# Optimization experiments

Measured on AMD Instinct MI355X. Metric: run time of the kernel, lower is better.

The kernel has to match this reference:

```python
import jax, jax.numpy as jnp
import numpy as np

D_MODEL = 1024
NUM_HEADS = 16
HEAD_DIM = D_MODEL // NUM_HEADS


def setup_inputs() -> dict:
    key = jax.random.key(0)
    ks = jax.random.split(key, 11)
    B, S = 4, 2048
    s = 1.0 / np.sqrt(D_MODEL)
    inp = {
        'query': jax.random.normal(ks[0], (B, S, D_MODEL), jnp.float32),
        'key': jax.random.normal(ks[1], (B, S, D_MODEL), jnp.float32),
        'value': jax.random.normal(ks[2], (B, S, D_MODEL), jnp.float32),
        'W_q': jax.random.normal(ks[3], (D_MODEL, D_MODEL), jnp.float32) * s,
        'b_q': jnp.zeros((D_MODEL,), jnp.float32),
        'W_k': jax.random.normal(ks[4], (D_MODEL, D_MODEL), jnp.float32) * s,
        'b_k': jnp.zeros((D_MODEL,), jnp.float32),
        'W_v': jax.random.normal(ks[5], (D_MODEL, D_MODEL), jnp.float32) * s,
        'b_v': jnp.zeros((D_MODEL,), jnp.float32),
        'W_o': jax.random.normal(ks[6], (D_MODEL, D_MODEL), jnp.float32) * s,
        'b_o': jnp.zeros((D_MODEL,), jnp.float32),
    }
    return inp


def reference(query, key, value, W_q, b_q, W_k, b_k, W_v, b_v, W_o, b_o):
    B, S, _ = query.shape
    # Linear projections (torch Linear: x @ W.T + b)
    Q = query @ W_q.T + b_q
    K = key @ W_k.T + b_k
    V = value @ W_v.T + b_v
    # [B, H, S, Dh]
    def split_heads(x):
        return x.reshape(B, -1, NUM_HEADS, HEAD_DIM).transpose(0, 2, 1, 3)
    Qh, Kh, Vh = split_heads(Q), split_heads(K), split_heads(V)
    scale = 1.0 / jnp.sqrt(jnp.float32(HEAD_DIM))
    scores = jnp.einsum('bhqd,bhkd->bhqk', Qh, Kh) * scale
    attn = jax.nn.softmax(scores, axis=-1)
    out = jnp.einsum('bhqk,bhkd->bhqd', attn, Vh)
    out = out.transpose(0, 2, 1, 3).reshape(B, S, D_MODEL)
    return out @ W_o.T + b_o
```

## Files before the change

kernel.cpp:

```cpp
#include <hip/hip_runtime.h>


#define BATCH 4
#define SEQ   2048
#define NH    16
#define DH    64
#define DM    1024
#define LOG2E 1.4426950408889634f
#define CSC   (0.125f * LOG2E)

typedef __attribute__((ext_vector_type(8))) short s16x8;
typedef __attribute__((ext_vector_type(4))) float f32x4;
typedef __attribute__((ext_vector_type(4))) unsigned int u32x4;
typedef const __attribute__((address_space(1))) unsigned int* gas1;
typedef __attribute__((address_space(3))) unsigned int* las3;

__device__ __forceinline__ unsigned short f2bf(float f) {
  unsigned int u = __float_as_uint(f);
  u += 0x7FFFu + ((u >> 16) & 1u);
  return (unsigned short)(u >> 16);
}

__device__ __forceinline__ unsigned int cvt_pk_bf16(float lo, float hi) {
  unsigned int r;
  asm("v_cvt_pk_bf16_f32 %0, %1, %2" : "=v"(r) : "v"(lo), "v"(hi));
  return r;
}

__device__ __forceinline__ f32x4 vmax4(f32x4 a, f32x4 b) {
  f32x4 r;
  r[0] = fmaxf(a[0], b[0]); r[1] = fmaxf(a[1], b[1]);
  r[2] = fmaxf(a[2], b[2]); r[3] = fmaxf(a[3], b[3]);
  return r;
}

__global__ __launch_bounds__(256) void cvt3_k(const float* __restrict__ s0,
                                              const float* __restrict__ s1,
                                              const float* __restrict__ s2,
                                              unsigned short* __restrict__ d0,
                                              unsigned short* __restrict__ d1,
                                              unsigned short* __restrict__ d2, int n4) {
  const float* s = blockIdx.y == 0 ? s0 : blockIdx.y == 1 ? s1 : s2;
  unsigned short* d = blockIdx.y == 0 ? d0 : blockIdx.y == 1 ? d1 : d2;
  int i = blockIdx.x * 256 + threadIdx.x;
  if (i < n4) {
    float4 v = ((const float4*)s)[i];
    ushort4 o;
    o.x = f2bf(v.x); o.y = f2bf(v.y); o.z = f2bf(v.z); o.w = f2bf(v.w);
    ((ushort4*)d)[i] = o;
  }
}

__global__ __launch_bounds__(256) void cvt4_k(const float* __restrict__ s0,
                                              const float* __restrict__ s1,
                                              const float* __restrict__ s2,
                                              const float* __restrict__ s3,
                                              unsigned short* __restrict__ d0,
                                              unsigned short* __restrict__ d1,
                                              unsigned short* __restrict__ d2,
                                              unsigned short* __restrict__ d3, int n4) {
  const float* s = blockIdx.y == 0 ? s0 : blockIdx.y == 1 ? s1 : blockIdx.y == 2 ? s2 : s3;
  unsigned short* d = blockIdx.y == 0 ? d0 : blockIdx.y == 1 ? d1 : blockIdx.y == 2 ? d2 : d3;
  int i = blockIdx.x * 256 + threadIdx.x;
  if (i < n4) {
    float4 v = ((const float4*)s)[i];
    ushort4 o;
    o.x = f2bf(v.x); o.y = f2bf(v.y); o.z = f2bf(v.z); o.w = f2bf(v.w);
    ((ushort4*)d)[i] = o;
  }
}

template<bool BIAS_ROW, bool OUT_F32>
__device__ __forceinline__ void gemm_core(const unsigned short* __restrict__ A,
                                          const unsigned short* __restrict__ Bm,
                                          const float* __restrict__ bias,
                                          void* __restrict__ Cout,
                                          int M, int N, int K, int tM, int tN,
                                          unsigned short* As, unsigned short* Bs) {
  const int tid = threadIdx.x;
  const int wave = tid >> 6, lane = tid & 63;
  const int lr = lane & 15, lh = lane >> 4;
  const int wm = (wave >> 1) * 64, wn = (wave & 1) * 64;
  f32x4 acc[4][4] = {};

  for (int k0 = 0; k0 < K; k0 += 64) {
    __syncthreads();
#pragma unroll
    for (int i = 0; i < 4; ++i) {
      const int slot = wave * 256 + i * 64 + lane;
      const int row = slot >> 3;
      const int cg = (slot & 7) ^ (row & 7);
      const unsigned short* ga = A  + (size_t)(tM * 128 + row) * K + k0 + cg * 8;
      const unsigned short* gb = Bm + (size_t)(tN * 128 + row) * K + k0 + cg * 8;
      __builtin_amdgcn_global_load_lds((gas1)ga, (las3)(As + (wave * 256 + i * 64) * 8), 16, 0, 0);
      __builtin_amdgcn_global_load_lds((gas1)gb, (las3)(Bs + (wave * 256 + i * 64) * 8), 16, 0, 0);
    }
    __syncthreads();

    s16x8 af[4][2], bfr[4][2];
#pragma unroll
    for (int mt = 0; mt < 4; ++mt) {
#pragma unroll
      for (int kt = 0; kt < 2; ++kt) {
        const int ra = wm + mt * 16 + lr;
        af[mt][kt] = *(const s16x8*)(As + ra * 64 + (((kt * 4 + lh) ^ (ra & 7)) * 8));
        const int rb = wn + mt * 16 + lr;
        bfr[mt][kt] = *(const s16x8*)(Bs + rb * 64 + (((kt * 4 + lh) ^ (rb & 7)) * 8));
      }
    }
#pragma unroll
    for (int mt = 0; mt < 4; ++mt) {
#pragma unroll
      for (int nt = 0; nt < 4; ++nt) {
        acc[mt][nt] = __builtin_amdgcn_mfma_f32_16x16x32_bf16(af[mt][0], bfr[nt][0], acc[mt][nt], 0, 0, 0);
        acc[mt][nt] = __builtin_amdgcn_mfma_f32_16x16x32_bf16(af[mt][1], bfr[nt][1], acc[mt][nt], 0, 0, 0);
      }
    }
  }

#pragma unroll
  for (int mt = 0; mt < 4; ++mt) {
#pragma unroll
    for (int nt = 0; nt < 4; ++nt) {
      const int row0 = tM * 128 + wm + mt * 16 + lh * 4;
      const int col  = tN * 128 + wn + nt * 16 + lr;
      const float bc = BIAS_ROW ? 0.f : bias[col];
#pragma unroll
      for (int r = 0; r < 4; ++r) {
        const float v = acc[mt][nt][r] + (BIAS_ROW ? bias[row0 + r] : bc);
        if (OUT_F32) ((float*)Cout)[(size_t)(row0 + r) * N + col] = v;
        else ((unsigned short*)Cout)[(size_t)(row0 + r) * N + col] = f2bf(v);
      }
    }
  }
}

template<bool BIAS_ROW, bool OUT_F32>
__global__ __launch_bounds__(256) void gemm_bt(const unsigned short* __restrict__ A,
                                               const unsigned short* __restrict__ Bm,
                                               const float* __restrict__ bias,
                                               void* __restrict__ Cout, int M, int N, int K) {
  __shared__ unsigned short As[128 * 64];
  __shared__ unsigned short Bs[128 * 64];
  gemm_core<BIAS_ROW, OUT_F32>(A, Bm, bias, Cout, M, N, K, blockIdx.y, blockIdx.x, As, Bs);
}

__global__ __launch_bounds__(256) void gemm_qk(const unsigned short* __restrict__ A0,
                                               const unsigned short* __restrict__ A1,
                                               const unsigned short* __restrict__ W0,
                                               const unsigned short* __restrict__ W1,
                                               const float* __restrict__ c0,
                                               const float* __restrict__ c1,
                                               void* __restrict__ C0, void* __restrict__ C1,
                                               int M, int N, int K) {
  __shared__ unsigned short As[128 * 64];
  __shared__ unsigned short Bs[128 * 64];
  if (blockIdx.z == 0)
    gemm_core<false, false>(A0, W0, c0, C0, M, N, K, blockIdx.y, blockIdx.x, As, Bs);
  else
    gemm_core<false, false>(A1, W1, c1, C1, M, N, K, blockIdx.y, blockIdx.x, As, Bs);
}

__global__ __launch_bounds__(256, 4) void attn_k(const unsigned short* __restrict__ Q,
                                                 const unsigned short* __restrict__ Kp,
                                                 const unsigned short* __restrict__ Vt,
                                                 unsigned short* __restrict__ AO) {
  __shared__ unsigned short Ks[2][64 * 64];
  __shared__ unsigned short Vs[2][64 * 64];
  __shared__ unsigned short Ps[4][16 * 64];
  const int tid = threadIdx.x;
  const int w = tid >> 6, lane = tid & 63;
  const int lr = lane & 15, lh = lane >> 4;
  const int sw = lr & 7;

  const int id = blockIdx.x;
  const int g  = (id & 7) * 128 + (id >> 3);
  const int qt = g & 15;
  const int hb = g >> 4;
  const int h = hb & 15, b = hb >> 4;

  s16x8 qf[2][2];
#pragma unroll
  for (int qb = 0; qb < 2; ++qb)
#pragma unroll
    for (int kt = 0; kt < 2; ++kt)
      qf[qb][kt] = *(const s16x8*)(Q + (size_t)(b * SEQ + qt * 128 + w * 32 + qb * 16 + lr) * DM
                                     + h * DH + kt * 32 + lh * 8);
  asm volatile("s_waitcnt vmcnt(0)" ::: "memory");
  __builtin_amdgcn_sched_barrier(0);

  f32x4 o[2][4] = {};
  float m_run[2] = {-1e30f, -1e30f};
  float l_run[2] = {0.f, 0.f};
  unsigned short* Pw = Ps[w];

  const unsigned short* Kbase = Kp + (size_t)b * SEQ * DM + h * DH;
  const unsigned short* Vbase = Vt + (size_t)h * DH * (BATCH * SEQ) + (size_t)b * SEQ;

  const int slot0 = w * 64 + lane, slot1 = 256 + w * 64 + lane;
  const int r0 = slot0 >> 3, c0 = (slot0 & 7) ^ (r0 & 7);
  const int r1 = slot1 >> 3, c1 = (slot1 & 7) ^ (r1 & 7);
  const unsigned short* gk0 = Kbase + (size_t)r0 * DM + c0 * 8;
  const unsigned short* gk1 = Kbase + (size_t)r1 * DM + c1 * 8;
  const unsigned short* gv0 = Vbase + (size_t)r0 * (BATCH * SEQ) + c0 * 8;
  const unsigned short* gv1 = Vbase + (size_t)r1 * (BATCH * SEQ) + c1 * 8;
  const int dst0 = (w * 64) * 8, dst1 = (256 + w * 64) * 8;

  auto stage = [&](int buf) {
    __builtin_amdgcn_global_load_lds((gas1)gk0, (las3)(&Ks[buf][dst0]), 16, 0, 0);
    __builtin_amdgcn_global_load_lds((gas1)gk1, (las3)(&Ks[buf][dst1]), 16, 0, 0);
    __builtin_amdgcn_global_load_lds((gas1)gv0, (las3)(&Vs[buf][dst0]), 16, 0, 0);
    __builtin_amdgcn_global_load_lds((gas1)gv1, (las3)(&Vs[buf][dst1]), 16, 0, 0);
    gk0 += 64 * DM; gk1 += 64 * DM; gv0 += 64; gv1 += 64;
  };

  stage(0);
  for (int t = 0; t < 32; ++t) {
    const int cur = t & 1;
    if (t < 31) {
      stage(cur ^ 1);
      asm volatile("s_waitcnt vmcnt(4)" ::: "memory");
    } else {
      asm volatile("s_waitcnt vmcnt(0)" ::: "memory");
    }
    __builtin_amdgcn_s_barrier();
    __builtin_amdgcn_sched_barrier(0);
    const unsigned short* Kc = Ks[cur];
    const unsigned short* Vc = Vs[cur];

    f32x4 s[2][4] = {};
    __builtin_amdgcn_s_setprio(1);
#pragma unroll
    for (int nt = 0; nt < 4; ++nt) {
#pragma unroll
      for (int kt = 0; kt < 2; ++kt) {
        const s16x8 kf = *(const s16x8*)(Kc + (nt * 16 + lr) * 64 + (((kt * 4 + lh) ^ sw) * 8));
        s[0][nt] = __builtin_amdgcn_mfma_f32_16x16x32_bf16(kf, qf[0][kt], s[0][nt], 0, 0, 0);
        s[1][nt] = __builtin_amdgcn_mfma_f32_16x16x32_bf16(kf, qf[1][kt], s[1][nt], 0, 0, 0);
      }
    }
    __builtin_amdgcn_s_setprio(0);

#pragma unroll
    for (int qb = 0; qb < 2; ++qb) {
      const f32x4 m03 = vmax4(vmax4(s[qb][0], s[qb][1]), vmax4(s[qb][2], s[qb][3]));
      float mx = fmaxf(fmaxf(m03[0], m03[1]), fmaxf(m03[2], m03[3]));
      mx = fmaxf(mx, __shfl_xor(mx, 16));
      mx = fmaxf(mx, __shfl_xor(mx, 32));
      if (!__all(mx - m_run[qb] <= 64.0f)) {
        const float al = __builtin_amdgcn_exp2f((m_run[qb] - mx) * CSC);
        m_run[qb] = mx;
        l_run[qb] *= al;
#pragma unroll
        for (int dt = 0; dt < 4; ++dt) o[qb][dt] *= al;
      }
      const float base = m_run[qb] * CSC;
#pragma unroll
      for (int nt = 0; nt < 4; ++nt)
#pragma unroll
        for (int r = 0; r < 4; ++r)
          s[qb][nt][r] = __builtin_amdgcn_exp2f(s[qb][nt][r] * CSC - base);
      const f32x4 st = (s[qb][0] + s[qb][1]) + (s[qb][2] + s[qb][3]);
      float rs = (st[0] + st[1]) + (st[2] + st[3]);
      rs += __shfl_xor(rs, 16);
      rs += __shfl_xor(rs, 32);
      l_run[qb] += rs;
    }

#pragma unroll
    for (int qb = 0; qb < 2; ++qb) {
#pragma unroll
      for (int nt = 0; nt < 4; ++nt) {
        uint2 wd;
        wd.x = cvt_pk_bf16(s[qb][nt][0], s[qb][nt][1]);
        wd.y = cvt_pk_bf16(s[qb][nt][2], s[qb][nt][3]);
        const int cp = (nt * 4 + lh + lr) & 15;
        *(uint2*)(Pw + lr * 64 + cp * 4) = wd;
      }
#pragma unroll
      for (int hf = 0; hf < 2; ++hf) {
        const int ca = (hf * 8 + lh * 2 + lr) & 15;
        const int cb = (hf * 8 + lh * 2 + 1 + lr) & 15;
        const uint2 lo = *(const uint2*)(Pw + lr * 64 + ca * 4);
        const uint2 hi = *(const uint2*)(Pw + lr * 64 + cb * 4);
        u32x4 pu;
        pu[0] = lo.x; pu[1] = lo.y; pu[2] = hi.x; pu[3] = hi.y;
        const s16x8 pf = __builtin_bit_cast(s16x8, pu);
        __builtin_amdgcn_s_setprio(1);
#pragma unroll
        for (int dt = 0; dt < 4; ++dt) {
          const s16x8 vf = *(const s16x8*)(Vc + (dt * 16 + lr) * 64 + (((hf * 4 + lh) ^ sw) * 8));
          o[qb][dt] = __builtin_amdgcn_mfma_f32_16x16x32_bf16(vf, pf, o[qb][dt], 0, 0, 0);
        }
        __builtin_amdgcn_s_setprio(0);
      }
    }
    __builtin_amdgcn_sched_barrier(0);
    __builtin_amdgcn_s_barrier();
  }

#pragma unroll
  for (int qb = 0; qb < 2; ++qb) {
    const float rl = __builtin_amdgcn_rcpf(l_run[qb]);
    unsigned short* orow = AO + (size_t)(b * SEQ + qt * 128 + w * 32 + qb * 16 + lr) * DM + h * DH;
#pragma unroll
    for (int dt = 0; dt < 4; ++dt) {
      *(unsigned int*)(orow + dt * 16 + lh * 4)     = cvt_pk_bf16(o[qb][dt][0] * rl, o[qb][dt][1] * rl);
      *(unsigned int*)(orow + dt * 16 + lh * 4 + 2) = cvt_pk_bf16(o[qb][dt][2] * rl, o[qb][dt][3] * rl);
    }
  }
}

extern "C" void kernel_launch(void* const* d_in, const int* in_sizes, int n_in,
                              void* d_out, int out_size, void* d_ws, size_t ws_size,
                              hipStream_t stream) {
  const float* q   = (const float*)d_in[0];
  const float* k   = (const float*)d_in[1];
  const float* v   = (const float*)d_in[2];
  const float* W_q = (const float*)d_in[3];
  const float* b_q = (const float*)d_in[4];
  const float* W_k = (const float*)d_in[5];
  const float* b_k = (const float*)d_in[6];
  const float* W_v = (const float*)d_in[7];
  const float* b_v = (const float*)d_in[8];
  const float* W_o = (const float*)d_in[9];
  const float* b_o = (const float*)d_in[10];

  const size_t SD  = (size_t)BATCH * SEQ * DM;
  const size_t SDB = SD * 2;
  const size_t D2  = (size_t)DM * DM;
  if (ws_size < 5 * SDB + D2 * 2) return;

  char* base = (char*)d_ws;
  unsigned short* B0 = (unsigned short*)(base);
  unsigned short* B1 = (unsigned short*)(base + 1 * SDB);
  unsigned short* B2 = (unsigned short*)(base + 2 * SDB);
  unsigned short* B3 = (unsigned short*)(base + 3 * SDB);
  unsigned short* B4 = (unsigned short*)(base + 4 * SDB);
  unsigned short* Wb = (unsigned short*)(base + 5 * SDB);

  unsigned short* dW0 = (unsigned short*)d_out;
  unsigned short* dW1 = dW0 + D2;
  unsigned short* dW2 = dW0 + 2 * D2;

  const int nSD4 = (int)(SD / 4), nD24 = (int)(D2 / 4);
  const dim3 blk(256);

  cvt3_k<<<dim3(nSD4 / 256, 3), blk, 0, stream>>>(q, k, v, B0, B1, B2, nSD4);
  cvt4_k<<<dim3(nD24 / 256, 4), blk, 0, stream>>>(W_q, W_k, W_v, W_o, dW0, dW1, dW2, Wb, nD24);
  gemm_qk<<<dim3(DM / 128, (BATCH * SEQ) / 128, 2), blk, 0, stream>>>(
      B0, B1, dW0, dW1, b_q, b_k, B3, B4, BATCH * SEQ, DM, DM);
  gemm_bt<true, false><<<dim3((BATCH * SEQ) / 128, DM / 128), blk, 0, stream>>>(
      dW2, B2, b_v, B1, DM, BATCH * SEQ, DM);
  attn_k<<<dim3(16 * NH * BATCH), blk, 0, stream>>>(B3, B4, B1, B0);
  gemm_bt<false, true><<<dim3(DM / 128, (BATCH * SEQ) / 128), blk, 0, stream>>>(
      B0, Wb, b_o, d_out, BATCH * SEQ, DM, DM);
}
```

Baseline: 230.0 us.

## Fold softmax scale into Q projection and hoist V fragment loads

Multiplies the Q projection output by the softmax scale times log2(e) in the GEMM epilogue, so the attention kernel drops the per-element multiply before exp2. The lazy-rescale threshold is adjusted to the new log2 units. V fragments are loaded from LDS once per tile and reused for both query blocks instead of being reloaded per block. P packing is moved next to the exp computation, and the KV loop is unrolled by two so buffer indices are compile-time constants. Storing pre-scaled Q in bf16 changes rounding slightly, and holding all V fragments at once raises register pressure.

```diff
diff --git a/kernel.cpp b/kernel.cpp
--- a/kernel.cpp
+++ b/kernel.cpp
@@ -7,7 +7,7 @@
 #define DH    64
 #define DM    1024
 #define LOG2E 1.4426950408889634f
-#define CSC   (0.125f * LOG2E)
+#define SCALE_Q (0.125f * LOG2E)
 
 typedef __attribute__((ext_vector_type(8))) short s16x8;
 typedef __attribute__((ext_vector_type(4))) float f32x4;
@@ -75,7 +75,7 @@
                                           const unsigned short* __restrict__ Bm,
                                           const float* __restrict__ bias,
                                           void* __restrict__ Cout,
-                                          int M, int N, int K, int tM, int tN,
+                                          int M, int N, int K, int tM, int tN, float scale,
                                           unsigned short* As, unsigned short* Bs) {
   const int tid = threadIdx.x;
   const int wave = tid >> 6, lane = tid & 63;
@@ -127,7 +127,7 @@
       const float bc = BIAS_ROW ? 0.f : bias[col];
 #pragma unroll
       for (int r = 0; r < 4; ++r) {
-        const float v = acc[mt][nt][r] + (BIAS_ROW ? bias[row0 + r] : bc);
+        const float v = (acc[mt][nt][r] + (BIAS_ROW ? bias[row0 + r] : bc)) * scale;
         if (OUT_F32) ((float*)Cout)[(size_t)(row0 + r) * N + col] = v;
         else ((unsigned short*)Cout)[(size_t)(row0 + r) * N + col] = f2bf(v);
       }
@@ -142,7 +142,7 @@
                                                void* __restrict__ Cout, int M, int N, int K) {
   __shared__ unsigned short As[128 * 64];
   __shared__ unsigned short Bs[128 * 64];
-  gemm_core<BIAS_ROW, OUT_F32>(A, Bm, bias, Cout, M, N, K, blockIdx.y, blockIdx.x, As, Bs);
+  gemm_core<BIAS_ROW, OUT_F32>(A, Bm, bias, Cout, M, N, K, blockIdx.y, blockIdx.x, 1.0f, As, Bs);
 }
 
 __global__ __launch_bounds__(256) void gemm_qk(const unsigned short* __restrict__ A0,
@@ -156,9 +156,9 @@
   __shared__ unsigned short As[128 * 64];
   __shared__ unsigned short Bs[128 * 64];
   if (blockIdx.z == 0)
-    gemm_core<false, false>(A0, W0, c0, C0, M, N, K, blockIdx.y, blockIdx.x, As, Bs);
+    gemm_core<false, false>(A0, W0, c0, C0, M, N, K, blockIdx.y, blockIdx.x, SCALE_Q, As, Bs);
   else
-    gemm_core<false, false>(A1, W1, c1, C1, M, N, K, blockIdx.y, blockIdx.x, As, Bs);
+    gemm_core<false, false>(A1, W1, c1, C1, M, N, K, blockIdx.y, blockIdx.x, 1.0f, As, Bs);
 }
 
 __global__ __launch_bounds__(256, 4) void attn_k(const unsigned short* __restrict__ Q,
@@ -214,19 +214,17 @@
     gk0 += 64 * DM; gk1 += 64 * DM; gv0 += 64; gv1 += 64;
   };
 
-  stage(0);
-  for (int t = 0; t < 32; ++t) {
-    const int cur = t & 1;
-    if (t < 31) {
-      stage(cur ^ 1);
+  auto tile = [&](int buf, bool prefetch) {
+    if (prefetch) {
+      stage(buf ^ 1);
       asm volatile("s_waitcnt vmcnt(4)" ::: "memory");
     } else {
       asm volatile("s_waitcnt vmcnt(0)" ::: "memory");
     }
     __builtin_amdgcn_s_barrier();
     __builtin_amdgcn_sched_barrier(0);
-    const unsigned short* Kc = Ks[cur];
-    const unsigned short* Vc = Vs[cur];
+    const unsigned short* Kc = Ks[buf];
+    const unsigned short* Vc = Vs[buf];
 
     f32x4 s[2][4] = {};
     __builtin_amdgcn_s_setprio(1);
@@ -241,42 +239,51 @@
     }
     __builtin_amdgcn_s_setprio(0);
 
+    s16x8 vf[8];
+#pragma unroll
+    for (int hf = 0; hf < 2; ++hf)
+#pragma unroll
+      for (int dt = 0; dt < 4; ++dt)
+        vf[hf * 4 + dt] = *(const s16x8*)(Vc + (dt * 16 + lr) * 64 + (((hf * 4 + lh) ^ sw) * 8));
+
+    uint2 pk[2][4];
 #pragma unroll
     for (int qb = 0; qb < 2; ++qb) {
       const f32x4 m03 = vmax4(vmax4(s[qb][0], s[qb][1]), vmax4(s[qb][2], s[qb][3]));
       float mx = fmaxf(fmaxf(m03[0], m03[1]), fmaxf(m03[2], m03[3]));
       mx = fmaxf(mx, __shfl_xor(mx, 16));
       mx = fmaxf(mx, __shfl_xor(mx, 32));
-      if (!__all(mx - m_run[qb] <= 64.0f)) {
-        const float al = __builtin_amdgcn_exp2f((m_run[qb] - mx) * CSC);
+      if (!__all(mx - m_run[qb] <= 11.5f)) {
+        const float al = __builtin_amdgcn_exp2f(m_run[qb] - mx);
         m_run[qb] = mx;
         l_run[qb] *= al;
 #pragma unroll
         for (int dt = 0; dt < 4; ++dt) o[qb][dt] *= al;
       }
-      const float base = m_run[qb] * CSC;
+      const float base = m_run[qb];
 #pragma unroll
       for (int nt = 0; nt < 4; ++nt)
 #pragma unroll
         for (int r = 0; r < 4; ++r)
-          s[qb][nt][r] = __builtin_amdgcn_exp2f(s[qb][nt][r] * CSC - base);
+          s[qb][nt][r] = __builtin_amdgcn_exp2f(s[qb][nt][r] - base);
       const f32x4 st = (s[qb][0] + s[qb][1]) + (s[qb][2] + s[qb][3]);
       float rs = (st[0] + st[1]) + (st[2] + st[3]);
       rs += __shfl_xor(rs, 16);
       rs += __shfl_xor(rs, 32);
       l_run[qb] += rs;
+#pragma unroll
+      for (int nt = 0; nt < 4; ++nt) {
+        pk[qb][nt].x = cvt_pk_bf16(s[qb][nt][0], s[qb][nt][1]);
+        pk[qb][nt].y = cvt_pk_bf16(s[qb][nt][2], s[qb][nt][3]);
+      }
     }
 
 #pragma unroll
     for (int qb = 0; qb < 2; ++qb) {
 #pragma unroll
-      for (int nt = 0; nt < 4; ++nt) {
-        uint2 wd;
-        wd.x = cvt_pk_bf16(s[qb][nt][0], s[qb][nt][1]);
-        wd.y = cvt_pk_bf16(s[qb][nt][2], s[qb][nt][3]);
-        const int cp = (nt * 4 + lh + lr) & 15;
-        *(uint2*)(Pw + lr * 64 + cp * 4) = wd;
-      }
+      for (int nt = 0; nt < 4; ++nt)
+        *(uint2*)(Pw + lr * 64 + (((nt * 4 + lh + lr) & 15) * 4)) = pk[qb][nt];
+      s16x8 pf[2];
 #pragma unroll
       for (int hf = 0; hf < 2; ++hf) {
         const int ca = (hf * 8 + lh * 2 + lr) & 15;
@@ -285,18 +292,24 @@
         const uint2 hi = *(const uint2*)(Pw + lr * 64 + cb * 4);
         u32x4 pu;
         pu[0] = lo.x; pu[1] = lo.y; pu[2] = hi.x; pu[3] = hi.y;
-        const s16x8 pf = __builtin_bit_cast(s16x8, pu);
-        __builtin_amdgcn_s_setprio(1);
-#pragma unroll
-        for (int dt = 0; dt < 4; ++dt) {
-          const s16x8 vf = *(const s16x8*)(Vc + (dt * 16 + lr) * 64 + (((hf * 4 + lh) ^ sw) * 8));
-          o[qb][dt] = __builtin_amdgcn_mfma_f32_16x16x32_bf16(vf, pf, o[qb][dt], 0, 0, 0);
-        }
-        __builtin_amdgcn_s_setprio(0);
-      }
+        pf[hf] = __builtin_bit_cast(s16x8, pu);
+      }
+      __builtin_amdgcn_s_setprio(1);
+#pragma unroll
+      for (int hf = 0; hf < 2; ++hf)
+#pragma unroll
+        for (int dt = 0; dt < 4; ++dt)
+          o[qb][dt] = __builtin_amdgcn_mfma_f32_16x16x32_bf16(vf[hf * 4 + dt], pf[hf], o[qb][dt], 0, 0, 0);
+      __builtin_amdgcn_s_setprio(0);
     }
     __builtin_amdgcn_sched_barrier(0);
     __builtin_amdgcn_s_barrier();
+  };
+
+  stage(0);
+  for (int tt = 0; tt < 16; ++tt) {
+    tile(0, true);
+    tile(1, tt != 15);
   }
 
 #pragma unroll
```

Result: slower. 312.1 us (+35.7%).
